# Kernel tuning notes

Measured on AMD Instinct MI355X. Metric: run time of the kernel, lower is better.

Reference implementation:

```python
import jax, jax.numpy as jnp
import numpy as np

START_IDX = 1  # undefined global `start_idx` in the source; fixed BOS id


def _lstm_gates(x_t, h, c, Wih, Whh, b):
    # PyTorch LSTM gate order: i, f, g, o
    gates = x_t @ Wih.T + h @ Whh.T + b
    i, f, g, o = jnp.split(gates, 4, axis=-1)
    c_new = jax.nn.sigmoid(f) * c + jax.nn.sigmoid(i) * jnp.tanh(g)
    h_new = jax.nn.sigmoid(o) * jnp.tanh(c_new)
    return h_new, c_new


def setup_inputs() -> dict:
    key = jax.random.key(0)
    ks = jax.random.split(key, 14)
    B, T, H, Vin, Vout = 64, 64, 512, 32000, 32000
    Hh = H // 2
    f = lambda k, shp, s=0.1: (jax.random.normal(k, shp) * s).astype(jnp.float32)
    return {
        "x": jax.random.randint(ks[0], (B, T), 0, Vin),
        "enc_emb": f(ks[1], (Vin, H), 0.2),
        "enc_wih_f": f(ks[2], (4 * Hh, H)),
        "enc_whh_f": f(ks[3], (4 * Hh, Hh)),
        "enc_b_f": jnp.zeros((4 * Hh,), jnp.float32),
        "enc_wih_b": f(ks[4], (4 * Hh, H)),
        "enc_whh_b": f(ks[5], (4 * Hh, Hh)),
        "enc_b_b": jnp.zeros((4 * Hh,), jnp.float32),
        "dec_emb": f(ks[6], (Vout, H), 0.2),
        "dec_wih": f(ks[7], (4 * H, H)),
        "dec_whh": f(ks[8], (4 * H, H)),
        "dec_b": jnp.zeros((4 * H,), jnp.float32),
        "clf_w": f(ks[9], (Vout, H), 0.2),
        "clf_b": jnp.zeros((Vout,), jnp.float32),
    }


def reference(x, enc_emb, enc_wih_f, enc_whh_f, enc_b_f,
              enc_wih_b, enc_whh_b, enc_b_b,
              dec_emb, dec_wih, dec_whh, dec_b, clf_w, clf_b):
    B, T = x.shape
    H = enc_emb.shape[1]
    Hh = H // 2

    # ---- Encoder: 1-layer bidirectional LSTM, hidden Hh per direction ----
    emb = enc_emb[x]                       # [B, T, H]
    xs = emb.transpose(1, 0, 2)            # [T, B, H] (scan over time)

    def run_dir(seq, Wih, Whh, b):
        def step(carry, xt):
            h, c = carry
            h, c = _lstm_gates(xt, h, c, Wih, Whh, b)
            return (h, c), None
        h0 = jnp.zeros((B, Hh), emb.dtype)
        (h, c), _ = jax.lax.scan(step, (h0, h0), seq)
        return h, c

    hf, cf = run_dir(xs, enc_wih_f, enc_whh_f, enc_b_f)
    hb, cb = run_dir(xs[::-1], enc_wih_b, enc_whh_b, enc_b_b)
    # hidden reshape in _forward_encoder: concat fwd/bwd final states -> [B, H]
    dec_h = jnp.concatenate([hf, hb], axis=-1)
    dec_c = jnp.concatenate([cf, cb], axis=-1)

    # ---- Decoder: greedy self-feeding loop for T-1 steps ----
    def dec_step(carry, _):
        h, c, y = carry
        e = dec_emb[y]                                  # [B, H]
        h, c = _lstm_gates(e, h, c, dec_wih, dec_whh, dec_b)
        logits = h @ clf_w.T + clf_b                    # [B, Vout]
        # argmax(softmax(logits)) == argmax(logits)
        y = jnp.argmax(logits, axis=-1)
        return (h, c, y), logits

    y0 = jnp.full((B,), START_IDX, dtype=x.dtype)
    _, logits = jax.lax.scan(dec_step, (dec_h, dec_c, y0), None, length=T - 1)
    # torch.cat(H, dim=2) with h.unsqueeze(2): [B, Vout, T-1]
    return logits.transpose(1, 2, 0)
```

## Files before the change

kernel.cpp:

```cpp
#include <hip/hip_runtime.h>
#include <math.h>

#define AM_PLAIN 0
#define AM_ENC   1
#define CM_PLAIN 0

typedef short bf16x8 __attribute__((ext_vector_type(8)));
typedef float f32x4 __attribute__((ext_vector_type(4)));

__device__ __forceinline__ float sigf(float x) { return 1.0f / (1.0f + expf(-x)); }

__device__ __forceinline__ unsigned short bf_rne(float f) {
  unsigned u = __float_as_uint(f);
  u += 0x7FFFu + ((u >> 16) & 1u);
  return (unsigned short)(u >> 16);
}
__device__ __forceinline__ float bf_f(unsigned short h) {
  return __uint_as_float(((unsigned)h) << 16);
}

template<int AMODE, int BTWO, int CMODE, int CDIR>
__global__ __launch_bounds__(256)
void gemm_k(const float* __restrict__ Ap, int lda,
            const float* __restrict__ emb,
            const int* __restrict__ xidx,
            const float* __restrict__ hbuf,
            const unsigned long long* __restrict__ cand_in, int nblk_cand, int step,
            const float* __restrict__ B0, const float* __restrict__ B1, int ldb,
            const float* __restrict__ bias,
            float* __restrict__ Cp, int ldc, long long zstride, int kper,
            unsigned long long* __restrict__ cand_out,
            float* __restrict__ dout, int tcol)
{
  __shared__ float As[32][68];
  __shared__ float Bs[32][68];
  __shared__ int ys[(AMODE == AM_PLAIN) ? 1 : 64];

  const int tid = threadIdx.x;
  const int tx = tid & 15, my = tid >> 4;
  const int n0 = tx * 4, m0 = my * 4;
  const int nbase = blockIdx.x * 64, mbase = blockIdx.y * 64;
  const int bz = blockIdx.z;

  if (AMODE == AM_ENC) {
    if (tid < 64) ys[tid] = xidx[tid * 64 + blockIdx.y];
  }
  if (AMODE != AM_PLAIN) __syncthreads();

  float acc[4][4];
#pragma unroll
  for (int i = 0; i < 4; ++i)
#pragma unroll
    for (int j = 0; j < 4; ++j) acc[i][j] = 0.0f;

  const int kbeg = bz * kper;
  const int lrow = tid >> 3, lk = (tid & 7) * 4;

  for (int kc = 0; kc < kper; kc += 32) {
    const int kg = kbeg + kc;
#pragma unroll
    for (int rr = 0; rr < 64; rr += 32) {
      const int row = lrow + rr;
      const float* ap;
      if (AMODE == AM_PLAIN) {
        ap = Ap + (size_t)(mbase + row) * lda + kg + lk;
      } else {
        ap = emb + (size_t)ys[row] * 512 + kg + lk;
      }
      const float4 v = *(const float4*)ap;
      As[lk + 0][row] = v.x; As[lk + 1][row] = v.y;
      As[lk + 2][row] = v.z; As[lk + 3][row] = v.w;

      const int n = nbase + row;
      const float* bp = B0 + (size_t)n * ldb + kg + lk;
      const float4 w = *(const float4*)bp;
      Bs[lk + 0][row] = w.x; Bs[lk + 1][row] = w.y;
      Bs[lk + 2][row] = w.z; Bs[lk + 3][row] = w.w;
    }
    __syncthreads();
#pragma unroll
    for (int k = 0; k < 32; ++k) {
      const float4 a = *(const float4*)&As[k][m0];
      const float4 b = *(const float4*)&Bs[k][n0];
      acc[0][0] += a.x * b.x; acc[0][1] += a.x * b.y; acc[0][2] += a.x * b.z; acc[0][3] += a.x * b.w;
      acc[1][0] += a.y * b.x; acc[1][1] += a.y * b.y; acc[1][2] += a.y * b.z; acc[1][3] += a.y * b.w;
      acc[2][0] += a.z * b.x; acc[2][1] += a.z * b.y; acc[2][2] += a.z * b.z; acc[2][3] += a.z * b.w;
      acc[3][0] += a.w * b.x; acc[3][1] += a.w * b.y; acc[3][2] += a.w * b.z; acc[3][3] += a.w * b.w;
    }
    __syncthreads();
  }

#pragma unroll
  for (int i = 0; i < 4; ++i) {
    const int m = mbase + m0 + i;
#pragma unroll
    for (int j = 0; j < 4; ++j) {
      const int n = nbase + n0 + j;
      float v = acc[i][j];
      if (bias) v += bias[n];
      Cp[bz * zstride + (size_t)m * ldc + n] = v;
    }
  }
}

__global__ __launch_bounds__(256)
void enc_step(const float* __restrict__ xwf, const float* __restrict__ xwb,
              const float* __restrict__ whhf, const float* __restrict__ whhb,
              const float* __restrict__ hin, float* __restrict__ hout,
              float* __restrict__ cbuf, int s)
{
  __shared__ float Hst[64][65];
  __shared__ float Ws[4][4][68];
  const int blk = blockIdx.x;
  const int d = blk >> 6, jt = blk & 63;
  const int j0 = jt * 4;
  const float* xw  = d ? xwb  : xwf;
  const float* whh = d ? whhb : whhf;
  const int t = d ? (63 - s) : s;
  const int tid = threadIdx.x;
  const int b = tid & 63, js = tid >> 6;
  const int j = j0 + js;

  float acc0 = 0.f, acc1 = 0.f, acc2 = 0.f, acc3 = 0.f;
  for (int kc = 0; kc < 256; kc += 64) {
    for (int q = js; q < 16; q += 4) {
      const float4 v = *(const float4*)&hin[(size_t)b * 512 + d * 256 + kc + q * 4];
      Hst[q * 4 + 0][b] = v.x; Hst[q * 4 + 1][b] = v.y;
      Hst[q * 4 + 2][b] = v.z; Hst[q * 4 + 3][b] = v.w;
    }
    {
      const int row = tid >> 4;
      const int kq = (tid & 15) * 4;
      const float4 v = *(const float4*)&whh[((size_t)((row >> 2) * 256 + j0 + (row & 3))) * 256 + kc + kq];
      Ws[row >> 2][row & 3][kq + 0] = v.x; Ws[row >> 2][row & 3][kq + 1] = v.y;
      Ws[row >> 2][row & 3][kq + 2] = v.z; Ws[row >> 2][row & 3][kq + 3] = v.w;
    }
    __syncthreads();
#pragma unroll
    for (int k = 0; k < 64; k += 4) {
      const float h0v = Hst[k][b], h1v = Hst[k + 1][b], h2v = Hst[k + 2][b], h3v = Hst[k + 3][b];
      const float4 w0 = *(const float4*)&Ws[0][js][k];
      const float4 w1 = *(const float4*)&Ws[1][js][k];
      const float4 w2 = *(const float4*)&Ws[2][js][k];
      const float4 w3 = *(const float4*)&Ws[3][js][k];
      acc0 += w0.x * h0v + w0.y * h1v + w0.z * h2v + w0.w * h3v;
      acc1 += w1.x * h0v + w1.y * h1v + w1.z * h2v + w1.w * h3v;
      acc2 += w2.x * h0v + w2.y * h1v + w2.z * h2v + w2.w * h3v;
      acc3 += w3.x * h0v + w3.y * h1v + w3.z * h2v + w3.w * h3v;
    }
    __syncthreads();
  }
  const float* xrow = xw + ((size_t)t * 64 + b) * 1024;
  const float gi = acc0 + xrow[0 * 256 + j];
  const float gf = acc1 + xrow[1 * 256 + j];
  const float gg = acc2 + xrow[2 * 256 + j];
  const float go = acc3 + xrow[3 * 256 + j];
  const size_t off = (size_t)b * 512 + d * 256 + j;
  const float cn = sigf(gf) * cbuf[off] + sigf(gi) * tanhf(gg);
  cbuf[off] = cn;
  hout[off] = sigf(go) * tanhf(cn);
}

__global__ void kinit(float* __restrict__ h0, float* __restrict__ c)
{
  const int i = blockIdx.x * 256 + threadIdx.x;
  if (i < 32768) { h0[i] = 0.f; c[i] = 0.f; }
}

__global__ __launch_bounds__(256)
void wconv(const float* __restrict__ p0, const float* __restrict__ p1,
           int ld, int split, int KC, short* __restrict__ frag, int total)
{
  const int i = blockIdx.x * 256 + threadIdx.x;
  if (i >= total) return;
  const int lane = i & 63;
  const int ck = i >> 6;
  const int kc = ck % KC;
  const int nt = ck / KC;
  const int n = nt * 16 + (lane & 15);
  const int k0 = kc * 32 + (lane >> 4) * 8;
  const float* src = (k0 < split) ? (p0 + (size_t)n * ld + k0)
                                  : (p1 + (size_t)n * ld + (k0 - split));
  const float4 v0 = *(const float4*)src;
  const float4 v1 = *(const float4*)(src + 4);
  const float x[8] = {v0.x, v0.y, v0.z, v0.w, v1.x, v1.y, v1.z, v1.w};
  bf16x8 vh, vl;
#pragma unroll
  for (int e = 0; e < 8; ++e) {
    const unsigned short h = bf_rne(x[e]);
    vh[e] = (short)h;
    vl[e] = (short)bf_rne(x[e] - bf_f(h));
  }
  const size_t base = (size_t)ck * 1024 + lane * 8;
  *(bf16x8*)(frag + base) = vh;
  *(bf16x8*)(frag + base + 512) = vl;
}

__global__ __launch_bounds__(256)
void h2frag(const float* __restrict__ h, short* __restrict__ frag)
{
  const int i = blockIdx.x * 256 + threadIdx.x;
  const int lane = i & 63;
  const int ck = i >> 6;
  const int b = (ck >> 4) * 16 + (lane & 15);
  const int k0 = (ck & 15) * 32 + (lane >> 4) * 8;
  const float* src = h + (size_t)b * 512 + k0;
  const float4 v0 = *(const float4*)src;
  const float4 v1 = *(const float4*)(src + 4);
  const float x[8] = {v0.x, v0.y, v0.z, v0.w, v1.x, v1.y, v1.z, v1.w};
  bf16x8 vh, vl;
#pragma unroll
  for (int e = 0; e < 8; ++e) {
    const unsigned short hh = bf_rne(x[e]);
    vh[e] = (short)hh;
    vl[e] = (short)bf_rne(x[e] - bf_f(hh));
  }
  const size_t base = (size_t)ck * 1024 + lane * 8;
  *(bf16x8*)(frag + base) = vh;
  *(bf16x8*)(frag + base + 512) = vl;
}

__global__ __launch_bounds__(256)
void demb2bf(const float* __restrict__ demb, short* __restrict__ debf)
{
  const int i = blockIdx.x * 256 + threadIdx.x;
  if (i >= 2048000) return;
  const int r = i >> 6;
  const int k0 = (i & 63) * 8;
  const float* src = demb + (size_t)r * 512 + k0;
  const float4 v0 = *(const float4*)src;
  const float4 v1 = *(const float4*)(src + 4);
  const float x[8] = {v0.x, v0.y, v0.z, v0.w, v1.x, v1.y, v1.z, v1.w};
  bf16x8 vh, vl;
#pragma unroll
  for (int e = 0; e < 8; ++e) {
    const unsigned short h = bf_rne(x[e]);
    vh[e] = (short)h;
    vl[e] = (short)bf_rne(x[e] - bf_f(h));
  }
  *(bf16x8*)(debf + (size_t)r * 1024 + k0) = vh;
  *(bf16x8*)(debf + (size_t)r * 1024 + 512 + k0) = vl;
}

#define NBLK_CLF 500

__global__ __launch_bounds__(1024)
void dec_gates(const short* __restrict__ debf,
               const short* __restrict__ gfrag,
               const unsigned long long* __restrict__ cand, int step,
               const float* __restrict__ db,
               const short* __restrict__ hfin, short* __restrict__ hfout,
               float* __restrict__ cbuf)
{
  __shared__ int ys[64];
  __shared__ unsigned long long red[16 * 64];
  __shared__ float gl[2][4][64][16];

  const int tid = threadIdx.x;
  const int lane = tid & 63, wv = tid >> 6;
  const int g = wv & 3, mh = (wv >> 2) & 1, kh = wv >> 3;
  const int j0 = blockIdx.x * 16;
  const int ntile = g * 32 + blockIdx.x;
  const int lrow = lane & 15, lq = lane >> 4;

  if (step == 0) {
    if (tid < 64) ys[tid] = 1;
  } else {
    const int b = tid & 63, slot = tid >> 6;
    unsigned long long mv = 0;
    for (int i2 = slot; i2 < NBLK_CLF; i2 += 16) {
      const unsigned long long v = cand[(size_t)i2 * 64 + b];
      mv = v > mv ? v : mv;
    }
    red[slot * 64 + b] = mv;
    __syncthreads();
    if (tid < 64) {
      unsigned long long m = red[tid];
#pragma unroll
      for (int s2 = 1; s2 < 16; ++s2) {
        const unsigned long long v = red[s2 * 64 + tid];
        m = v > m ? v : m;
      }
      ys[tid] = (int)(0xFFFFFFFFu - (unsigned)(m & 0xFFFFFFFFull));
    }
  }
  __syncthreads();

  f32x4 acc[2];
#pragma unroll
  for (int mtl = 0; mtl < 2; ++mtl) acc[mtl] = (f32x4){0.f, 0.f, 0.f, 0.f};

  if (kh == 0) {
    for (int kc = 0; kc < 16; ++kc) {
      const short* wb = gfrag + ((size_t)(ntile * 32 + kc)) * 1024 + lane * 8;
      const bf16x8 bhi = *(const bf16x8*)wb;
      const bf16x8 blo = *(const bf16x8*)(wb + 512);
      const int k0 = kc * 32 + lq * 8;
#pragma unroll
      for (int mtl = 0; mtl < 2; ++mtl) {
        const int b = (mh * 2 + mtl) * 16 + lrow;
        const short* ap = debf + (size_t)ys[b] * 1024 + k0;
        const bf16x8 ahi = *(const bf16x8*)ap;
        const bf16x8 alo = *(const bf16x8*)(ap + 512);
        acc[mtl] = __builtin_amdgcn_mfma_f32_16x16x32_bf16(ahi, bhi, acc[mtl], 0, 0, 0);
        acc[mtl] = __builtin_amdgcn_mfma_f32_16x16x32_bf16(alo, bhi, acc[mtl], 0, 0, 0);
        acc[mtl] = __builtin_amdgcn_mfma_f32_16x16x32_bf16(ahi, blo, acc[mtl], 0, 0, 0);
      }
    }
  } else {
    for (int kc = 16; kc < 32; ++kc) {
      const short* wb = gfrag + ((size_t)(ntile * 32 + kc)) * 1024 + lane * 8;
      const bf16x8 bhi = *(const bf16x8*)wb;
      const bf16x8 blo = *(const bf16x8*)(wb + 512);
#pragma unroll
      for (int mtl = 0; mtl < 2; ++mtl) {
        const int mt = mh * 2 + mtl;
        const short* ab = hfin + ((size_t)(mt * 16 + (kc - 16))) * 1024 + lane * 8;
        const bf16x8 ahi = *(const bf16x8*)ab;
        const bf16x8 alo = *(const bf16x8*)(ab + 512);
        acc[mtl] = __builtin_amdgcn_mfma_f32_16x16x32_bf16(ahi, bhi, acc[mtl], 0, 0, 0);
        acc[mtl] = __builtin_amdgcn_mfma_f32_16x16x32_bf16(alo, bhi, acc[mtl], 0, 0, 0);
        acc[mtl] = __builtin_amdgcn_mfma_f32_16x16x32_bf16(ahi, blo, acc[mtl], 0, 0, 0);
      }
    }
  }

#pragma unroll
  for (int mtl = 0; mtl < 2; ++mtl)
#pragma unroll
    for (int r = 0; r < 4; ++r) {
      const int b = (mh * 2 + mtl) * 16 + lq * 4 + r;
      gl[kh][g][b][lrow] = acc[mtl][r];
    }
  __syncthreads();

  {
    const int b = tid >> 4, jl = tid & 15;
    const int j = j0 + jl;
    const float gi = gl[0][0][b][jl] + gl[1][0][b][jl] + db[j];
    const float gf = gl[0][1][b][jl] + gl[1][1][b][jl] + db[512 + j];
    const float gg = gl[0][2][b][jl] + gl[1][2][b][jl] + db[1024 + j];
    const float go = gl[0][3][b][jl] + gl[1][3][b][jl] + db[1536 + j];
    const size_t off = (size_t)b * 512 + j;
    const float cn = sigf(gf) * cbuf[off] + sigf(gi) * tanhf(gg);
    cbuf[off] = cn;
    const float hn = sigf(go) * tanhf(cn);
    const unsigned short hh = bf_rne(hn);
    const unsigned short hl2 = bf_rne(hn - bf_f(hh));
    const int mt = b >> 4;
    const int kc = j >> 5;
    const size_t base = ((size_t)(mt * 16 + kc)) * 1024 + ((((j & 31) >> 3) * 16) + (b & 15)) * 8 + (j & 7);
    hfout[base] = (short)hh;
    hfout[base + 512] = (short)hl2;
  }
}

template<int DIRECT>
__global__ __launch_bounds__(256)
void dec_clf(const short* __restrict__ hfrag, const short* __restrict__ wfrag,
             const float* __restrict__ clfb,
             float* __restrict__ dst, int tcol,
             unsigned long long* __restrict__ cand_out)
{
  __shared__ unsigned long long cl[4][64];
  const int tid = threadIdx.x;
  const int lane = tid & 63, wv = tid >> 6;
  const int ntile = blockIdx.x * 4 + wv;
  const int lrow = lane & 15, lq = lane >> 4;

  f32x4 acc[4];
#pragma unroll
  for (int mt = 0; mt < 4; ++mt) acc[mt] = (f32x4){0.f, 0.f, 0.f, 0.f};

#pragma unroll 2
  for (int kc = 0; kc < 16; ++kc) {
    const short* wb = wfrag + ((size_t)(ntile * 16 + kc)) * 1024 + lane * 8;
    const bf16x8 bhi = *(const bf16x8*)wb;
    const bf16x8 blo = *(const bf16x8*)(wb + 512);
#pragma unroll
    for (int mt = 0; mt < 4; ++mt) {
      const short* ab = hfrag + ((size_t)(mt * 16 + kc)) * 1024 + lane * 8;
      const bf16x8 ahi = *(const bf16x8*)ab;
      const bf16x8 alo = *(const bf16x8*)(ab + 512);
      acc[mt] = __builtin_amdgcn_mfma_f32_16x16x32_bf16(ahi, bhi, acc[mt], 0, 0, 0);
      acc[mt] = __builtin_amdgcn_mfma_f32_16x16x32_bf16(alo, bhi, acc[mt], 0, 0, 0);
      acc[mt] = __builtin_amdgcn_mfma_f32_16x16x32_bf16(ahi, blo, acc[mt], 0, 0, 0);
    }
  }

  const int v = ntile * 16 + lrow;
  const float bias = clfb[v];
#pragma unroll
  for (int mt = 0; mt < 4; ++mt) {
#pragma unroll
    for (int r = 0; r < 4; ++r) {
      const float val = acc[mt][r] + bias;
      const int b = mt * 16 + lq * 4 + r;
      if (DIRECT) __builtin_nontemporal_store(val, dst + ((size_t)b * 32000 + v) * 63 + tcol);
      else        __builtin_nontemporal_store(val, dst + (size_t)b * 32000 + v);
      unsigned u = __float_as_uint(val);
      u ^= (u & 0x80000000u) ? 0xFFFFFFFFu : 0x80000000u;
      unsigned long long p = ((unsigned long long)u << 32) |
                             (unsigned long long)(0xFFFFFFFFu - (unsigned)v);
#pragma unroll
      for (int m2 = 1; m2 < 16; m2 <<= 1) {
        const unsigned long long o = __shfl_xor(p, m2);
        p = o > p ? o : p;
      }
      if (lrow == 0) cl[wv][b] = p;
    }
  }
  __syncthreads();
  if (tid < 64) {
    unsigned long long m = cl[0][tid];
    const unsigned long long v1 = cl[1][tid];
    const unsigned long long v2 = cl[2][tid];
    const unsigned long long v3 = cl[3][tid];
    m = v1 > m ? v1 : m; m = v2 > m ? v2 : m; m = v3 > m ? v3 : m;
    cand_out[(size_t)blockIdx.x * 64 + tid] = m;
  }
}

__global__ __launch_bounds__(256)
void transpose_out(const float* __restrict__ ls, float* __restrict__ out)
{
  __shared__ float tile[128 * 63];
  const int b = blockIdx.y;
  const int v0 = blockIdx.x * 128;
  for (int idx = threadIdx.x; idx < 128 * 63; idx += 256) {
    const int t = idx >> 7, v = idx & 127;
    tile[v * 63 + t] = ls[((size_t)t * 64 + b) * 32000 + v0 + v];
  }
  __syncthreads();
  float4* o4 = (float4*)(out + ((size_t)b * 32000 + v0) * 63);
  const float4* t4 = (const float4*)tile;
  for (int i = threadIdx.x; i < (128 * 63) / 4; i += 256) o4[i] = t4[i];
}

extern "C" void kernel_launch(void* const* d_in, const int* in_sizes, int n_in,
                              void* d_out, int out_size, void* d_ws, size_t ws_size,
                              hipStream_t stream)
{
  const int*   x       = (const int*)d_in[0];
  const float* enc_emb = (const float*)d_in[1];
  const float* ewih_f  = (const float*)d_in[2];
  const float* ewhh_f  = (const float*)d_in[3];
  const float* eb_f    = (const float*)d_in[4];
  const float* ewih_b  = (const float*)d_in[5];
  const float* ewhh_b  = (const float*)d_in[6];
  const float* eb_b    = (const float*)d_in[7];
  const float* demb    = (const float*)d_in[8];
  const float* dwih    = (const float*)d_in[9];
  const float* dwhh    = (const float*)d_in[10];
  const float* db      = (const float*)d_in[11];
  const float* clfw    = (const float*)d_in[12];
  const float* clfb    = (const float*)d_in[13];
  float* out = (float*)d_out;
  float* ws  = (float*)d_ws;

  float* xwf = ws;
  float* xwb = xwf + 4194304;
  float* h0  = xwb + 4194304;
  float* h1  = h0 + 32768;
  float* cbf = h1 + 32768;
  unsigned long long* cand = (unsigned long long*)(cbf + 32768);
  short* wfrag  = (short*)(cbf + 32768 + 64000);
  short* gfrag  = wfrag + 32768000;
  short* hfragA = gfrag + 4194304;
  short* hfragB = hfragA + 65536;
  short* debf   = hfragB + 65536;
  float* ls = (float*)(debf + 32768000);
  const size_t need_f = 4194304ull * 2 + 32768ull * 3 + 64000ull
                      + 16384000ull + 2097152ull + 32768ull * 2
                      + 16384000ull + 129024000ull;
  const bool wspath = ws_size >= need_f * sizeof(float);

  kinit<<<dim3(128), dim3(256), 0, stream>>>(h0, cbf);

  wconv<<<dim3(8000), dim3(256), 0, stream>>>(clfw, clfw, 512, 512, 16, wfrag, 2048000);
  wconv<<<dim3(1024), dim3(256), 0, stream>>>(dwih, dwhh, 512, 512, 32, gfrag, 262144);
  demb2bf<<<dim3(8000), dim3(256), 0, stream>>>(demb, debf);

  dim3 gx(16, 64, 1);
  gemm_k<AM_ENC, 0, CM_PLAIN, 0><<<gx, 256, 0, stream>>>(
      nullptr, 0, enc_emb, x, nullptr, nullptr, 0, 0,
      ewih_f, nullptr, 512, eb_f, xwf, 1024, 0, 512, nullptr, nullptr, 0);
  gemm_k<AM_ENC, 0, CM_PLAIN, 0><<<gx, 256, 0, stream>>>(
      nullptr, 0, enc_emb, x, nullptr, nullptr, 0, 0,
      ewih_b, nullptr, 512, eb_b, xwb, 1024, 0, 512, nullptr, nullptr, 0);

  for (int s = 0; s < 64; ++s) {
    float* hin  = (s & 1) ? h1 : h0;
    float* hout = (s & 1) ? h0 : h1;
    enc_step<<<dim3(128), dim3(256), 0, stream>>>(xwf, xwb, ewhh_f, ewhh_b, hin, hout, cbf, s);
  }
  h2frag<<<dim3(16), dim3(256), 0, stream>>>(h0, hfragA);

  for (int t = 0; t < 63; ++t) {
    const short* hin = (t & 1) ? hfragB : hfragA;
    short* hout      = (t & 1) ? hfragA : hfragB;
    dec_gates<<<dim3(32), dim3(1024), 0, stream>>>(debf, gfrag, cand, t, db, hin, hout, cbf);
    if (wspath) {
      dec_clf<0><<<dim3(NBLK_CLF), dim3(256), 0, stream>>>(
          hout, wfrag, clfb, ls + (size_t)t * 2048000, t, cand);
    } else {
      dec_clf<1><<<dim3(NBLK_CLF), dim3(256), 0, stream>>>(
          hout, wfrag, clfb, out, t, cand);
    }
  }

  if (wspath) transpose_out<<<dim3(250, 64), 256, 0, stream>>>(ls, out);
}
```

Before: 4.378 ms.

## Fuse encoder LSTM time loop into a persistent MFMA kernel per direction

```diff
diff --git a/kernel.cpp b/kernel.cpp
--- a/kernel.cpp
+++ b/kernel.cpp
@@ -103,68 +103,105 @@
   }
 }
 
-__global__ __launch_bounds__(256)
-void enc_step(const float* __restrict__ xwf, const float* __restrict__ xwb,
-              const float* __restrict__ whhf, const float* __restrict__ whhb,
-              const float* __restrict__ hin, float* __restrict__ hout,
-              float* __restrict__ cbuf, int s)
-{
-  __shared__ float Hst[64][65];
-  __shared__ float Ws[4][4][68];
-  const int blk = blockIdx.x;
-  const int d = blk >> 6, jt = blk & 63;
-  const int j0 = jt * 4;
-  const float* xw  = d ? xwb  : xwf;
-  const float* whh = d ? whhb : whhf;
-  const int t = d ? (63 - s) : s;
+__global__ __launch_bounds__(512)
+void enc_fused(const float* __restrict__ xwf, const float* __restrict__ xwb,
+               const short* __restrict__ whhfF, const short* __restrict__ whhfB,
+               float* __restrict__ hfinal, float* __restrict__ cfinal)
+{
+  __shared__ short hfr[32768];
+
+  const int d = blockIdx.x;
+  const float* xw = d ? xwb : xwf;
+  const short* wf = d ? whhfB : whhfF;
   const int tid = threadIdx.x;
-  const int b = tid & 63, js = tid >> 6;
-  const int j = j0 + js;
-
-  float acc0 = 0.f, acc1 = 0.f, acc2 = 0.f, acc3 = 0.f;
-  for (int kc = 0; kc < 256; kc += 64) {
-    for (int q = js; q < 16; q += 4) {
-      const float4 v = *(const float4*)&hin[(size_t)b * 512 + d * 256 + kc + q * 4];
-      Hst[q * 4 + 0][b] = v.x; Hst[q * 4 + 1][b] = v.y;
-      Hst[q * 4 + 2][b] = v.z; Hst[q * 4 + 3][b] = v.w;
-    }
-    {
-      const int row = tid >> 4;
-      const int kq = (tid & 15) * 4;
-      const float4 v = *(const float4*)&whh[((size_t)((row >> 2) * 256 + j0 + (row & 3))) * 256 + kc + kq];
-      Ws[row >> 2][row & 3][kq + 0] = v.x; Ws[row >> 2][row & 3][kq + 1] = v.y;
-      Ws[row >> 2][row & 3][kq + 2] = v.z; Ws[row >> 2][row & 3][kq + 3] = v.w;
-    }
+  const int lane = tid & 63, wv = tid >> 6;
+  const int lrow = lane & 15, lq = lane >> 4;
+
+  for (int i = tid; i < 16384; i += 512) ((int*)hfr)[i] = 0;
+  __syncthreads();
+
+  float c[2][16];
+#pragma unroll
+  for (int jtl = 0; jtl < 2; ++jtl)
+#pragma unroll
+    for (int el = 0; el < 16; ++el) c[jtl][el] = 0.f;
+
+  for (int s = 0; s < 64; ++s) {
+    const int t = d ? (63 - s) : s;
+    float hnew[2][16];
+
+#pragma unroll
+    for (int jtl = 0; jtl < 2; ++jtl) {
+      const int jt = wv + jtl * 8;
+      f32x4 acc[4][4];
+#pragma unroll
+      for (int g = 0; g < 4; ++g)
+#pragma unroll
+        for (int mt = 0; mt < 4; ++mt)
+#pragma unroll
+          for (int r = 0; r < 4; ++r) {
+            const int b = mt * 16 + lq * 4 + r;
+            acc[g][mt][r] = xw[((size_t)(t * 64 + b)) * 1024 + g * 256 + jt * 16 + lrow];
+          }
+#pragma unroll
+      for (int kc = 0; kc < 8; ++kc) {
+        bf16x8 ah[4], al[4];
+#pragma unroll
+        for (int mt = 0; mt < 4; ++mt) {
+          const short* ab = hfr + ((mt * 8 + kc) * 2) * 512 + lane * 8;
+          ah[mt] = *(const bf16x8*)ab;
+          al[mt] = *(const bf16x8*)(ab + 512);
+        }
+#pragma unroll
+        for (int g = 0; g < 4; ++g) {
+          const short* wb = wf + ((size_t)((g * 16 + jt) * 8 + kc)) * 1024 + lane * 8;
+          const bf16x8 bhi = *(const bf16x8*)wb;
+          const bf16x8 blo = *(const bf16x8*)(wb + 512);
+#pragma unroll
+          for (int mt = 0; mt < 4; ++mt) {
+            acc[g][mt] = __builtin_amdgcn_mfma_f32_16x16x32_bf16(ah[mt], bhi, acc[g][mt], 0, 0, 0);
+            acc[g][mt] = __builtin_amdgcn_mfma_f32_16x16x32_bf16(al[mt], bhi, acc[g][mt], 0, 0, 0);
+            acc[g][mt] = __builtin_amdgcn_mfma_f32_16x16x32_bf16(ah[mt], blo, acc[g][mt], 0, 0, 0);
+          }
+        }
+      }
+#pragma unroll
+      for (int el = 0; el < 16; ++el) {
+        const int mt = el >> 2, r = el & 3;
+        const float gi = acc[0][mt][r];
+        const float gf = acc[1][mt][r];
+        const float gg = acc[2][mt][r];
+        const float go = acc[3][mt][r];
+        const float cn = sigf(gf) * c[jtl][el] + sigf(gi) * tanhf(gg);
+        c[jtl][el] = cn;
+        hnew[jtl][el] = sigf(go) * tanhf(cn);
+      }
+    }
+
     __syncthreads();
 #pragma unroll
-    for (int k = 0; k < 64; k += 4) {
-      const float h0v = Hst[k][b], h1v = Hst[k + 1][b], h2v = Hst[k + 2][b], h3v = Hst[k + 3][b];
-      const float4 w0 = *(const float4*)&Ws[0][js][k];
-      const float4 w1 = *(const float4*)&Ws[1][js][k];
-      const float4 w2 = *(const float4*)&Ws[2][js][k];
-      const float4 w3 = *(const float4*)&Ws[3][js][k];
-      acc0 += w0.x * h0v + w0.y * h1v + w0.z * h2v + w0.w * h3v;
-      acc1 += w1.x * h0v + w1.y * h1v + w1.z * h2v + w1.w * h3v;
-      acc2 += w2.x * h0v + w2.y * h1v + w2.z * h2v + w2.w * h3v;
-      acc3 += w3.x * h0v + w3.y * h1v + w3.z * h2v + w3.w * h3v;
+    for (int jtl = 0; jtl < 2; ++jtl) {
+      const int jt = wv + jtl * 8;
+#pragma unroll
+      for (int el = 0; el < 16; ++el) {
+        const int mt = el >> 2, r = el & 3;
+        const int b = mt * 16 + lq * 4 + r;
+        const int j = jt * 16 + lrow;
+        const float hn = hnew[jtl][el];
+        const unsigned short hh = bf_rne(hn);
+        const unsigned short ll = bf_rne(hn - bf_f(hh));
+        const int base = ((mt * 8 + (j >> 5)) * 2) * 512 + (((j >> 3) & 3) * 16 + (b & 15)) * 8 + (j & 7);
+        hfr[base] = (short)hh;
+        hfr[base + 512] = (short)ll;
+        if (s == 63) {
+          const size_t off = (size_t)b * 512 + d * 256 + j;
+          hfinal[off] = hn;
+          cfinal[off] = c[jtl][el];
+        }
+      }
     }
     __syncthreads();
   }
-  const float* xrow = xw + ((size_t)t * 64 + b) * 1024;
-  const float gi = acc0 + xrow[0 * 256 + j];
-  const float gf = acc1 + xrow[1 * 256 + j];
-  const float gg = acc2 + xrow[2 * 256 + j];
-  const float go = acc3 + xrow[3 * 256 + j];
-  const size_t off = (size_t)b * 512 + d * 256 + j;
-  const float cn = sigf(gf) * cbuf[off] + sigf(gi) * tanhf(gg);
-  cbuf[off] = cn;
-  hout[off] = sigf(go) * tanhf(cn);
-}
-
-__global__ void kinit(float* __restrict__ h0, float* __restrict__ c)
-{
-  const int i = blockIdx.x * 256 + threadIdx.x;
-  if (i < 32768) { h0[i] = 0.f; c[i] = 0.f; }
 }
 
 __global__ __launch_bounds__(256)
@@ -469,14 +506,16 @@
   short* hfragA = gfrag + 4194304;
   short* hfragB = hfragA + 65536;
   short* debf   = hfragB + 65536;
-  float* ls = (float*)(debf + 32768000);
+  short* ehfF   = debf + 32768000;
+  short* ehfB   = ehfF + 524288;
+  float* ls = (float*)(ehfB + 524288);
   const size_t need_f = 4194304ull * 2 + 32768ull * 3 + 64000ull
                       + 16384000ull + 2097152ull + 32768ull * 2
-                      + 16384000ull + 129024000ull;
+                      + 16384000ull + 262144ull * 2 + 129024000ull;
   const bool wspath = ws_size >= need_f * sizeof(float);
 
-  kinit<<<dim3(128), dim3(256), 0, stream>>>(h0, cbf);
-
+  wconv<<<dim3(128), dim3(256), 0, stream>>>(ewhh_f, ewhh_f, 256, 256, 8, ehfF, 32768);
+  wconv<<<dim3(128), dim3(256), 0, stream>>>(ewhh_b, ewhh_b, 256, 256, 8, ehfB, 32768);
   wconv<<<dim3(8000), dim3(256), 0, stream>>>(clfw, clfw, 512, 512, 16, wfrag, 2048000);
   wconv<<<dim3(1024), dim3(256), 0, stream>>>(dwih, dwhh, 512, 512, 32, gfrag, 262144);
   demb2bf<<<dim3(8000), dim3(256), 0, stream>>>(demb, debf);
@@ -489,11 +528,8 @@
       nullptr, 0, enc_emb, x, nullptr, nullptr, 0, 0,
       ewih_b, nullptr, 512, eb_b, xwb, 1024, 0, 512, nullptr, nullptr, 0);
 
-  for (int s = 0; s < 64; ++s) {
-    float* hin  = (s & 1) ? h1 : h0;
-    float* hout = (s & 1) ? h0 : h1;
-    enc_step<<<dim3(128), dim3(256), 0, stream>>>(xwf, xwb, ewhh_f, ewhh_b, hin, hout, cbf, s);
-  }
+  enc_fused<<<dim3(2), dim3(512), 0, stream>>>(xwf, xwb, ehfF, ehfB, h0, cbf);
+
   h2frag<<<dim3(16), dim3(256), 0, stream>>>(h0, hfragA);
 
   for (int t = 0; t < 63; ++t) {
```

Result: slower. 6.204 ms (+41.7%).

## Use split-bf16 MFMA for encoder recurrent matmul with pre-fragmented weights

Applied to the files above, without the earlier changes.

```diff
diff --git a/kernel.cpp b/kernel.cpp
--- a/kernel.cpp
+++ b/kernel.cpp
@@ -103,68 +103,87 @@
   }
 }
 
-__global__ __launch_bounds__(256)
-void enc_step(const float* __restrict__ xwf, const float* __restrict__ xwb,
-              const float* __restrict__ whhf, const float* __restrict__ whhb,
-              const float* __restrict__ hin, float* __restrict__ hout,
-              float* __restrict__ cbuf, int s)
-{
-  __shared__ float Hst[64][65];
-  __shared__ float Ws[4][4][68];
+__global__ __launch_bounds__(1024)
+void enc_mstep(const float* __restrict__ xwf, const float* __restrict__ xwb,
+               const short* __restrict__ whhfF, const short* __restrict__ whhfB,
+               const short* __restrict__ hin, short* __restrict__ hout,
+               float* __restrict__ cbuf, float* __restrict__ hfinal, int s)
+{
+  __shared__ float gl[2][4][64][16];
+
   const int blk = blockIdx.x;
-  const int d = blk >> 6, jt = blk & 63;
-  const int j0 = jt * 4;
-  const float* xw  = d ? xwb  : xwf;
-  const float* whh = d ? whhb : whhf;
+  const int d = blk >> 4;
+  const int jb = blk & 15;
+  const int j0 = jb * 16;
+  const float* xw = d ? xwb : xwf;
+  const short* wf = d ? whhfB : whhfF;
+  const short* hi_ = hin + d * 32768;
+  short* ho_ = hout + d * 32768;
   const int t = d ? (63 - s) : s;
+
   const int tid = threadIdx.x;
-  const int b = tid & 63, js = tid >> 6;
-  const int j = j0 + js;
-
-  float acc0 = 0.f, acc1 = 0.f, acc2 = 0.f, acc3 = 0.f;
-  for (int kc = 0; kc < 256; kc += 64) {
-    for (int q = js; q < 16; q += 4) {
-      const float4 v = *(const float4*)&hin[(size_t)b * 512 + d * 256 + kc + q * 4];
-      Hst[q * 4 + 0][b] = v.x; Hst[q * 4 + 1][b] = v.y;
-      Hst[q * 4 + 2][b] = v.z; Hst[q * 4 + 3][b] = v.w;
-    }
-    {
-      const int row = tid >> 4;
-      const int kq = (tid & 15) * 4;
-      const float4 v = *(const float4*)&whh[((size_t)((row >> 2) * 256 + j0 + (row & 3))) * 256 + kc + kq];
-      Ws[row >> 2][row & 3][kq + 0] = v.x; Ws[row >> 2][row & 3][kq + 1] = v.y;
-      Ws[row >> 2][row & 3][kq + 2] = v.z; Ws[row >> 2][row & 3][kq + 3] = v.w;
-    }
-    __syncthreads();
-#pragma unroll
-    for (int k = 0; k < 64; k += 4) {
-      const float h0v = Hst[k][b], h1v = Hst[k + 1][b], h2v = Hst[k + 2][b], h3v = Hst[k + 3][b];
-      const float4 w0 = *(const float4*)&Ws[0][js][k];
-      const float4 w1 = *(const float4*)&Ws[1][js][k];
-      const float4 w2 = *(const float4*)&Ws[2][js][k];
-      const float4 w3 = *(const float4*)&Ws[3][js][k];
-      acc0 += w0.x * h0v + w0.y * h1v + w0.z * h2v + w0.w * h3v;
-      acc1 += w1.x * h0v + w1.y * h1v + w1.z * h2v + w1.w * h3v;
-      acc2 += w2.x * h0v + w2.y * h1v + w2.z * h2v + w2.w * h3v;
-      acc3 += w3.x * h0v + w3.y * h1v + w3.z * h2v + w3.w * h3v;
-    }
-    __syncthreads();
-  }
-  const float* xrow = xw + ((size_t)t * 64 + b) * 1024;
-  const float gi = acc0 + xrow[0 * 256 + j];
-  const float gf = acc1 + xrow[1 * 256 + j];
-  const float gg = acc2 + xrow[2 * 256 + j];
-  const float go = acc3 + xrow[3 * 256 + j];
-  const size_t off = (size_t)b * 512 + d * 256 + j;
-  const float cn = sigf(gf) * cbuf[off] + sigf(gi) * tanhf(gg);
-  cbuf[off] = cn;
-  hout[off] = sigf(go) * tanhf(cn);
-}
-
-__global__ void kinit(float* __restrict__ h0, float* __restrict__ c)
+  const int lane = tid & 63, wv = tid >> 6;
+  const int g = wv & 3, mh = (wv >> 2) & 1, kh = wv >> 3;
+  const int lrow = lane & 15, lq = lane >> 4;
+  const int ntile = g * 16 + jb;
+
+  f32x4 acc[2];
+#pragma unroll
+  for (int mtl = 0; mtl < 2; ++mtl) acc[mtl] = (f32x4){0.f, 0.f, 0.f, 0.f};
+
+#pragma unroll
+  for (int kk = 0; kk < 4; ++kk) {
+    const int kc = kh * 4 + kk;
+    const short* wb = wf + ((size_t)(ntile * 8 + kc)) * 1024 + lane * 8;
+    const bf16x8 bhi = *(const bf16x8*)wb;
+    const bf16x8 blo = *(const bf16x8*)(wb + 512);
+#pragma unroll
+    for (int mtl = 0; mtl < 2; ++mtl) {
+      const int mt = mh * 2 + mtl;
+      const short* ab = hi_ + ((size_t)(mt * 8 + kc)) * 1024 + lane * 8;
+      const bf16x8 ahi = *(const bf16x8*)ab;
+      const bf16x8 alo = *(const bf16x8*)(ab + 512);
+      acc[mtl] = __builtin_amdgcn_mfma_f32_16x16x32_bf16(ahi, bhi, acc[mtl], 0, 0, 0);
+      acc[mtl] = __builtin_amdgcn_mfma_f32_16x16x32_bf16(alo, bhi, acc[mtl], 0, 0, 0);
+      acc[mtl] = __builtin_amdgcn_mfma_f32_16x16x32_bf16(ahi, blo, acc[mtl], 0, 0, 0);
+    }
+  }
+
+#pragma unroll
+  for (int mtl = 0; mtl < 2; ++mtl)
+#pragma unroll
+    for (int r = 0; r < 4; ++r) {
+      const int b = (mh * 2 + mtl) * 16 + lq * 4 + r;
+      gl[kh][g][b][lrow] = acc[mtl][r];
+    }
+  __syncthreads();
+
+  {
+    const int b = tid >> 4, jl = tid & 15;
+    const int j = j0 + jl;
+    const float* xrow = xw + ((size_t)(t * 64 + b)) * 1024;
+    const float gi = gl[0][0][b][jl] + gl[1][0][b][jl] + xrow[0 * 256 + j];
+    const float gf = gl[0][1][b][jl] + gl[1][1][b][jl] + xrow[1 * 256 + j];
+    const float gg = gl[0][2][b][jl] + gl[1][2][b][jl] + xrow[2 * 256 + j];
+    const float go = gl[0][3][b][jl] + gl[1][3][b][jl] + xrow[3 * 256 + j];
+    const size_t off = (size_t)b * 512 + d * 256 + j;
+    const float cn = sigf(gf) * cbuf[off] + sigf(gi) * tanhf(gg);
+    cbuf[off] = cn;
+    const float hn = sigf(go) * tanhf(cn);
+    const unsigned short hh = bf_rne(hn);
+    const unsigned short ll = bf_rne(hn - bf_f(hh));
+    const int mt = b >> 4;
+    const int base = ((mt * 8 + (j >> 5)) * 2) * 512 + (((j >> 3) & 3) * 16 + (b & 15)) * 8 + (j & 7);
+    ho_[base] = (short)hh;
+    ho_[base + 512] = (short)ll;
+    if (s == 63) hfinal[off] = hn;
+  }
+}
+
+__global__ void kinit2(float* __restrict__ c, int* __restrict__ he)
 {
   const int i = blockIdx.x * 256 + threadIdx.x;
-  if (i < 32768) { h0[i] = 0.f; c[i] = 0.f; }
+  if (i < 32768) { c[i] = 0.f; he[i] = 0; }
 }
 
 __global__ __launch_bounds__(256)
@@ -469,14 +488,20 @@
   short* hfragA = gfrag + 4194304;
   short* hfragB = hfragA + 65536;
   short* debf   = hfragB + 65536;
-  float* ls = (float*)(debf + 32768000);
+  short* ehfF   = debf + 32768000;
+  short* ehfB   = ehfF + 524288;
+  short* he0    = ehfB + 524288;
+  short* he1    = he0 + 65536;
+  float* ls = (float*)(he1 + 65536);
   const size_t need_f = 4194304ull * 2 + 32768ull * 3 + 64000ull
                       + 16384000ull + 2097152ull + 32768ull * 2
-                      + 16384000ull + 129024000ull;
+                      + 16384000ull + 262144ull * 2 + 32768ull * 2 + 129024000ull;
   const bool wspath = ws_size >= need_f * sizeof(float);
 
-  kinit<<<dim3(128), dim3(256), 0, stream>>>(h0, cbf);
-
+  kinit2<<<dim3(128), dim3(256), 0, stream>>>(cbf, (int*)he0);
+
+  wconv<<<dim3(128), dim3(256), 0, stream>>>(ewhh_f, ewhh_f, 256, 256, 8, ehfF, 32768);
+  wconv<<<dim3(128), dim3(256), 0, stream>>>(ewhh_b, ewhh_b, 256, 256, 8, ehfB, 32768);
   wconv<<<dim3(8000), dim3(256), 0, stream>>>(clfw, clfw, 512, 512, 16, wfrag, 2048000);
   wconv<<<dim3(1024), dim3(256), 0, stream>>>(dwih, dwhh, 512, 512, 32, gfrag, 262144);
   demb2bf<<<dim3(8000), dim3(256), 0, stream>>>(demb, debf);
@@ -490,10 +515,12 @@
       ewih_b, nullptr, 512, eb_b, xwb, 1024, 0, 512, nullptr, nullptr, 0);
 
   for (int s = 0; s < 64; ++s) {
-    float* hin  = (s & 1) ? h1 : h0;
-    float* hout = (s & 1) ? h0 : h1;
-    enc_step<<<dim3(128), dim3(256), 0, stream>>>(xwf, xwb, ewhh_f, ewhh_b, hin, hout, cbf, s);
-  }
+    const short* hin = (s & 1) ? he1 : he0;
+    short* hout      = (s & 1) ? he0 : he1;
+    enc_mstep<<<dim3(32), dim3(1024), 0, stream>>>(
+        xwf, xwb, ehfF, ehfB, hin, hout, cbf, h0, s);
+  }
+
   h2frag<<<dim3(16), dim3(256), 0, stream>>>(h0, hfragA);
 
   for (int t = 0; t < 63; ++t) {
```

After: 3.922 ms. 10.4% less time.
